# Optimization experiments

Hardware: AMD Instinct MI355X
Metric: run time of the kernel (lower is better)

## Reference

```python
import jax, jax.numpy as jnp
import numpy as np

D_MODEL = 1024
D_FF = 4096
NUM_EXPERTS = 8
TOP_K = 2


def setup_inputs() -> dict:
    key = jax.random.key(0)
    ks = jax.random.split(key, 7)
    s = 1.0 / np.sqrt(D_MODEL)
    sf = 1.0 / np.sqrt(D_FF)
    x = jax.random.normal(ks[0], (4, 2048, D_MODEL), dtype=jnp.float32)
    gate_w = jax.random.uniform(ks[1], (D_MODEL, NUM_EXPERTS), minval=-s, maxval=s, dtype=jnp.float32)
    gate_b = jnp.zeros((NUM_EXPERTS,), dtype=jnp.float32)
    w1 = jax.random.uniform(ks[2], (NUM_EXPERTS, D_MODEL, D_FF), minval=-s, maxval=s, dtype=jnp.float32)
    b1 = jax.random.uniform(ks[3], (NUM_EXPERTS, D_FF), minval=-s, maxval=s, dtype=jnp.float32)
    w2 = jax.random.uniform(ks[4], (NUM_EXPERTS, D_FF, D_MODEL), minval=-sf, maxval=sf, dtype=jnp.float32)
    b2 = jax.random.uniform(ks[5], (NUM_EXPERTS, D_MODEL), minval=-sf, maxval=sf, dtype=jnp.float32)
    return {"x": x, "gate_w": gate_w, "gate_b": gate_b, "w1": w1, "b1": b1, "w2": w2, "b2": b2}


def reference(x, gate_w, gate_b, w1, b1, w2, b2):
    # Router: softmax over experts, then top-k with renormalization.
    router_logits = jnp.einsum('bsd,de->bse', x, gate_w) + gate_b  # [B,S,E]
    router_probs = jax.nn.softmax(router_logits, axis=-1)
    topk_probs, topk_idx = jax.lax.top_k(router_probs, TOP_K)      # [B,S,K]
    topk_probs = topk_probs / jnp.sum(topk_probs, axis=-1, keepdims=True)

    # Dense combine weights: comb[b,s,e] = sum_k topk_probs[b,s,k] * (topk_idx[b,s,k]==e)
    one_hot = jax.nn.one_hot(topk_idx, NUM_EXPERTS, dtype=x.dtype)  # [B,S,K,E]
    comb = jnp.einsum('bsk,bske->bse', topk_probs, one_hot)         # [B,S,E]

    # Loop over the small fixed expert set; weight unselected experts by 0.
    out = jnp.zeros_like(x)
    for e in range(NUM_EXPERTS):
        h = jax.nn.relu(jnp.einsum('bsd,df->bsf', x, w1[e]) + b1[e])
        y = jnp.einsum('bsf,fd->bsd', h, w2[e]) + b2[e]
        out = out + comb[..., e:e + 1] * y

    # Routing statistics (same math as the torch module).
    expert_usage = jnp.mean(one_hot, axis=(0, 1, 2))  # fraction of (token,k) slots per expert
    avg_probs = jnp.mean(router_probs, axis=(0, 1))
    load_balance_loss = jnp.var(avg_probs, ddof=1)    # torch.var is unbiased by default
    return out, expert_usage, load_balance_loss
```

## Files before the change

### kernel.cpp

```cpp
#include <hip/hip_runtime.h>
#include <hip/hip_bf16.h>
#include <stdint.h>

#define D_MODEL 1024
#define D_FF    4096
#define NE      8
#define NTOK    8192
#define OUT_MAIN (NTOK * D_MODEL)

typedef float f32x4 __attribute__((ext_vector_type(4)));
typedef short s16x8 __attribute__((ext_vector_type(8)));

struct __align__(8) bh4 { __hip_bfloat16 x, y, z, w; };

static const size_t OFF_E12  = 4096;
static const size_t OFF_PFR  = 36864;
static const size_t OFF_ATOK = 102400;
static const size_t OFF_AP   = 167936;
static const size_t OFF_XB   = 262144;
static const size_t OFF_W1T  = OFF_XB  + (size_t)NTOK * D_MODEL * 2;
static const size_t OFF_W2T  = OFF_W1T + (size_t)NE * D_MODEL * D_FF * 2;
static const size_t OFF_H    = OFF_W2T + (size_t)NE * D_MODEL * D_FF * 2;

__device__ inline void gll16(const void* g, void* lds) {
  __builtin_amdgcn_global_load_lds((__attribute__((address_space(1))) void*)g,
                                   (__attribute__((address_space(3))) void*)lds,
                                   16, 0, 0);
}

__global__ __launch_bounds__(256) void cvt_transpose_kernel(
    const float* __restrict__ src, __hip_bfloat16* __restrict__ dst, int K, int N)
{
  __shared__ __hip_bfloat16 tile[64][68];
  const int e = blockIdx.z;
  const float* s = src + (size_t)e * K * N;
  __hip_bfloat16* d = dst + (size_t)e * K * N;
  const int n0 = blockIdx.x * 64, k0 = blockIdx.y * 64;
  const int t = threadIdx.x;
#pragma unroll
  for (int i = 0; i < 4; ++i) {
    int q = i * 256 + t;
    int r = q >> 4, c4 = (q & 15) * 4;
    float4 v = *(const float4*)(s + (size_t)(k0 + r) * N + n0 + c4);
    tile[r][c4 + 0] = __float2bfloat16(v.x);
    tile[r][c4 + 1] = __float2bfloat16(v.y);
    tile[r][c4 + 2] = __float2bfloat16(v.z);
    tile[r][c4 + 3] = __float2bfloat16(v.w);
  }
  __syncthreads();
  const int n = t >> 2, c = (t & 3) * 16;
  __align__(16) __hip_bfloat16 tmp[16];
#pragma unroll
  for (int j = 0; j < 16; ++j) tmp[j] = tile[c + j][n];
  uint4* tv = (uint4*)tmp;
  __hip_bfloat16* dp = d + (size_t)(n0 + n) * K + k0 + c;
  ((uint4*)dp)[0] = tv[0];
  ((uint4*)dp)[1] = tv[1];
}

__global__ __launch_bounds__(256) void router_kernel(
    const float* __restrict__ x, const float* __restrict__ gw, const float* __restrict__ gb,
    __hip_bfloat16* __restrict__ xb, int* __restrict__ e12, float2* __restrict__ pfr,
    int* __restrict__ cnt, float* __restrict__ probsum)
{
  const int l = threadIdx.x & 63;
  const int t = blockIdx.x * 4 + (threadIdx.x >> 6);
  const float4* xr = (const float4*)(x + (size_t)t * D_MODEL);
  bh4* xbr = (bh4*)(xb + (size_t)t * D_MODEL);
  float a[8] = {0, 0, 0, 0, 0, 0, 0, 0};
#pragma unroll
  for (int c = 0; c < 4; ++c) {
    int idx = c * 64 + l;
    float4 v = xr[idx];
    bh4 hb;
    hb.x = __float2bfloat16(v.x); hb.y = __float2bfloat16(v.y);
    hb.z = __float2bfloat16(v.z); hb.w = __float2bfloat16(v.w);
    xbr[idx] = hb;
    const float* g = gw + (size_t)idx * 32;
#pragma unroll
    for (int j = 0; j < 4; ++j) {
      float xv = (&v.x)[j];
#pragma unroll
      for (int e = 0; e < 8; ++e) a[e] = fmaf(xv, g[j * 8 + e], a[e]);
    }
  }
#pragma unroll
  for (int e = 0; e < 8; ++e) {
    float s = a[e];
#pragma unroll
    for (int off = 32; off > 0; off >>= 1) s += __shfl_xor(s, off, 64);
    a[e] = s + gb[e];
  }
  float m = a[0];
#pragma unroll
  for (int e = 1; e < 8; ++e) m = fmaxf(m, a[e]);
  float p[8], s = 0.f;
#pragma unroll
  for (int e = 0; e < 8; ++e) { p[e] = expf(a[e] - m); s += p[e]; }
  float inv = 1.0f / s;
#pragma unroll
  for (int e = 0; e < 8; ++e) p[e] *= inv;
  int e1 = 0; float p1 = p[0];
#pragma unroll
  for (int e = 1; e < 8; ++e) if (p[e] > p1) { p1 = p[e]; e1 = e; }
  int e2 = (e1 == 0) ? 1 : 0; float p2 = p[e2];
#pragma unroll
  for (int e = 0; e < 8; ++e) if (e != e1 && p[e] > p2) { p2 = p[e]; e2 = e; }

  if (l < 8) unsafeAtomicAdd(probsum + l, p[l]);
  if (l == 0) {
    float rs = 1.0f / (p1 + p2);
    e12[t] = e1 | (e2 << 8);
    pfr[t] = make_float2(p1 * rs, p2 * rs);
    atomicAdd(cnt + e1, 1);
    atomicAdd(cnt + e2, 1);
  }
}

__global__ void finalize_kernel(int* __restrict__ ctrl, float* __restrict__ probsum,
                                float* __restrict__ out_tail)
{
  if (threadIdx.x != 0) return;
  int off = 0;
  float avg[8]; float mean = 0.f;
#pragma unroll
  for (int e = 0; e < 8; ++e) {
    int c = ctrl[e];
    ctrl[8 + e]  = off;
    ctrl[16 + e] = off;
    off += c;
    out_tail[e] = (float)c * (1.0f / 16384.0f);
    avg[e] = probsum[e] * (1.0f / 8192.0f);
    mean += avg[e];
  }
  mean *= 0.125f;
  float v = 0.f;
#pragma unroll
  for (int e = 0; e < 8; ++e) { float d = avg[e] - mean; v += d * d; }
  out_tail[8] = v * (1.0f / 7.0f);
}

__global__ __launch_bounds__(256) void scatter_kernel(
    const int* __restrict__ e12, const float2* __restrict__ pfr,
    int* __restrict__ cursor, int* __restrict__ atok, float* __restrict__ ap)
{
  int t = blockIdx.x * 256 + threadIdx.x;
  int ee = e12[t];
  float2 p = pfr[t];
  int pos0 = atomicAdd(cursor + (ee & 0xff), 1);
  atok[pos0] = t; ap[pos0] = p.x;
  int pos1 = atomicAdd(cursor + (ee >> 8), 1);
  atok[pos1] = t; ap[pos1] = p.y;
}

template <bool G1>
__global__ __launch_bounds__(256) void moe_gemm_kernel(
    const __hip_bfloat16* __restrict__ A, const __hip_bfloat16* __restrict__ Bw,
    const float* __restrict__ bias, __hip_bfloat16* __restrict__ Hout,
    float* __restrict__ Oout, const int* __restrict__ ctrl,
    const int* __restrict__ atok, const float* __restrict__ ap)
{
  constexpr int KD = G1 ? D_MODEL : D_FF;
  constexpr int ND = G1 ? D_FF : D_MODEL;
  constexpr int KITERS = KD / 64;
  const int e = blockIdx.z;
  const int cte = ctrl[e];
  const int mt = blockIdx.y;
  if (mt * 128 >= cte) return;
  const int n0 = blockIdx.x * 128;
  const int slot0 = ctrl[16 + e] + mt * 128;
  int cntLoc = cte - mt * 128; if (cntLoc > 128) cntLoc = 128;

  __shared__ ushort As[128 * 64];
  __shared__ ushort Bs[128 * 64];

  const int t = threadIdx.x, l = t & 63, w = t >> 6;

  const ushort* ag[4];
  const ushort* bg[4];
#pragma unroll
  for (int i = 0; i < 4; ++i) {
    int q = i * 256 + t;
    int row = q >> 3, cl = q & 7, cg = cl ^ (row & 7);
    int rr = row < cntLoc ? row : 0;
    size_t arow;
    if constexpr (G1) arow = (size_t)atok[slot0 + rr] * D_MODEL;
    else              arow = (size_t)(slot0 + rr) * D_FF;
    ag[i] = (const ushort*)A + arow + cg * 8;
    bg[i] = (const ushort*)Bw + (size_t)e * ND * KD + (size_t)(n0 + row) * KD + cg * 8;
  }

  f32x4 acc[4][4] = {};
  const int wm = w & 1, wn = w >> 1;
  const int ml = l & 15, kg = l >> 4;

  for (int kt = 0; kt < KITERS; ++kt) {
#pragma unroll
    for (int i = 0; i < 4; ++i) {
      gll16(ag[i], &As[(i * 256 + w * 64) * 8]);
      ag[i] += 64;
    }
#pragma unroll
    for (int i = 0; i < 4; ++i) {
      gll16(bg[i], &Bs[(i * 256 + w * 64) * 8]);
      bg[i] += 64;
    }
    __syncthreads();
#pragma unroll
    for (int ks = 0; ks < 2; ++ks) {
      s16x8 af[4], bf[4];
#pragma unroll
      for (int mi = 0; mi < 4; ++mi) {
        int row = wm * 64 + mi * 16 + ml;
        int c = ks * 4 + kg;
        af[mi] = *(const s16x8*)&As[row * 64 + ((c ^ (row & 7)) * 8)];
      }
#pragma unroll
      for (int ni = 0; ni < 4; ++ni) {
        int row = wn * 64 + ni * 16 + ml;
        int c = ks * 4 + kg;
        bf[ni] = *(const s16x8*)&Bs[row * 64 + ((c ^ (row & 7)) * 8)];
      }
#pragma unroll
      for (int mi = 0; mi < 4; ++mi)
#pragma unroll
        for (int ni = 0; ni < 4; ++ni)
          acc[mi][ni] = __builtin_amdgcn_mfma_f32_16x16x32_bf16(af[mi], bf[ni], acc[mi][ni], 0, 0, 0);
    }
    __syncthreads();
  }

  const int lr = kg * 4, lc = ml;
  if constexpr (G1) {
#pragma unroll
    for (int ni = 0; ni < 4; ++ni) {
      int col = n0 + wn * 64 + ni * 16 + lc;
      float bv = bias[(size_t)e * ND + col];
#pragma unroll
      for (int mi = 0; mi < 4; ++mi) {
#pragma unroll
        for (int r = 0; r < 4; ++r) {
          int rl = wm * 64 + mi * 16 + lr + r;
          if (rl < cntLoc) {
            float vv = fmaxf(acc[mi][ni][r] + bv, 0.0f);
            Hout[(size_t)(slot0 + rl) * D_FF + col] = __float2bfloat16(vv);
          }
        }
      }
    }
  } else {
    float bv[4];
#pragma unroll
    for (int ni = 0; ni < 4; ++ni)
      bv[ni] = bias[(size_t)e * ND + n0 + wn * 64 + ni * 16 + lc];
#pragma unroll
    for (int mi = 0; mi < 4; ++mi) {
#pragma unroll
      for (int r = 0; r < 4; ++r) {
        int rl = wm * 64 + mi * 16 + lr + r;
        if (rl < cntLoc) {
          int slot = slot0 + rl;
          float p = ap[slot];
          float* orow = Oout + (size_t)atok[slot] * D_MODEL + n0;
#pragma unroll
          for (int ni = 0; ni < 4; ++ni) {
            int colL = wn * 64 + ni * 16 + lc;
            unsafeAtomicAdd(orow + colL, p * (acc[mi][ni][r] + bv[ni]));
          }
        }
      }
    }
  }
}

extern "C" void kernel_launch(void* const* d_in, const int* in_sizes, int n_in,
                              void* d_out, int out_size, void* d_ws, size_t ws_size,
                              hipStream_t stream)
{
  const float* x  = (const float*)d_in[0];
  const float* gw = (const float*)d_in[1];
  const float* gb = (const float*)d_in[2];
  const float* w1 = (const float*)d_in[3];
  const float* b1 = (const float*)d_in[4];
  const float* w2 = (const float*)d_in[5];
  const float* b2 = (const float*)d_in[6];
  float* out = (float*)d_out;
  char* ws = (char*)d_ws;

  int*    ctrl    = (int*)ws;
  float*  probsum = (float*)ws + 24;
  int*    e12  = (int*)(ws + OFF_E12);
  float2* pfr  = (float2*)(ws + OFF_PFR);
  int*    atok = (int*)(ws + OFF_ATOK);
  float*  ap   = (float*)(ws + OFF_AP);
  __hip_bfloat16* xb   = (__hip_bfloat16*)(ws + OFF_XB);
  __hip_bfloat16* w1t  = (__hip_bfloat16*)(ws + OFF_W1T);
  __hip_bfloat16* w2t  = (__hip_bfloat16*)(ws + OFF_W2T);
  __hip_bfloat16* hbuf = (__hip_bfloat16*)(ws + OFF_H);

  hipMemsetAsync(d_out, 0, (size_t)out_size * sizeof(float), stream);
  hipMemsetAsync(d_ws, 0, 4096, stream);

  cvt_transpose_kernel<<<dim3(D_FF / 64, D_MODEL / 64, NE), 256, 0, stream>>>(w1, w1t, D_MODEL, D_FF);
  cvt_transpose_kernel<<<dim3(D_MODEL / 64, D_FF / 64, NE), 256, 0, stream>>>(w2, w2t, D_FF, D_MODEL);
  router_kernel<<<NTOK / 4, 256, 0, stream>>>(x, gw, gb, xb, e12, pfr, ctrl, probsum);
  finalize_kernel<<<1, 64, 0, stream>>>(ctrl, probsum, out + OUT_MAIN);
  scatter_kernel<<<NTOK / 256, 256, 0, stream>>>(e12, pfr, ctrl + 8, atok, ap);
  moe_gemm_kernel<true ><<<dim3(D_FF / 128, 64, NE), 256, 0, stream>>>(xb, w1t, b1, hbuf, nullptr, ctrl, atok, ap);
  moe_gemm_kernel<false><<<dim3(D_MODEL / 128, 64, NE), 256, 0, stream>>>(hbuf, w2t, b2, nullptr, out, ctrl, atok, ap);
}
```

Before: 1.160 ms.

## Split-K the second expert GEMM and make token scatter deterministic

The down-projection GEMM is split into two K halves, each a separate block that atomically adds into the output, with the bias applied only by the first half. This doubles the block count for the smaller-N GEMM and should improve occupancy. Router statistics now use per-block partial sums, and a ballot-based count/place pass replaces the global atomic scatter, which also removes the workspace memset. The split-K path doubles the atomic traffic to the output in exchange for more parallelism.

```diff
diff --git a/kernel.cpp b/kernel.cpp
--- a/kernel.cpp
+++ b/kernel.cpp
@@ -13,14 +13,14 @@
 
 struct __align__(8) bh4 { __hip_bfloat16 x, y, z, w; };
 
-static const size_t OFF_E12  = 4096;
-static const size_t OFF_PFR  = 36864;
-static const size_t OFF_ATOK = 102400;
-static const size_t OFF_AP   = 167936;
-static const size_t OFF_XB   = 262144;
-static const size_t OFF_W1T  = OFF_XB  + (size_t)NTOK * D_MODEL * 2;
-static const size_t OFF_W2T  = OFF_W1T + (size_t)NE * D_MODEL * D_FF * 2;
-static const size_t OFF_H    = OFF_W2T + (size_t)NE * D_MODEL * D_FF * 2;
+static const size_t OFF_E12   = 4096;
+static const size_t OFF_PFR   = 36864;
+static const size_t OFF_ATOK  = 102400;
+static const size_t OFF_AP    = 167936;
+static const size_t OFF_XB    = 262144;
+static const size_t OFF_W1T   = OFF_XB  + (size_t)NTOK * D_MODEL * 2;
+static const size_t OFF_W2T   = OFF_W1T + (size_t)NE * D_MODEL * D_FF * 2;
+static const size_t OFF_H     = OFF_W2T + (size_t)NE * D_MODEL * D_FF * 2;
 
 __device__ inline void gll16(const void* g, void* lds) {
   __builtin_amdgcn_global_load_lds((__attribute__((address_space(1))) void*)g,
@@ -61,10 +61,12 @@
 __global__ __launch_bounds__(256) void router_kernel(
     const float* __restrict__ x, const float* __restrict__ gw, const float* __restrict__ gb,
     __hip_bfloat16* __restrict__ xb, int* __restrict__ e12, float2* __restrict__ pfr,
-    int* __restrict__ cnt, float* __restrict__ probsum)
-{
+    float* __restrict__ blkps)
+{
+  __shared__ float lps[4][8];
   const int l = threadIdx.x & 63;
-  const int t = blockIdx.x * 4 + (threadIdx.x >> 6);
+  const int w = threadIdx.x >> 6;
+  const int t = blockIdx.x * 4 + w;
   const float4* xr = (const float4*)(x + (size_t)t * D_MODEL);
   bh4* xbr = (bh4*)(xb + (size_t)t * D_MODEL);
   float a[8] = {0, 0, 0, 0, 0, 0, 0, 0};
@@ -107,50 +109,106 @@
 #pragma unroll
   for (int e = 0; e < 8; ++e) if (e != e1 && p[e] > p2) { p2 = p[e]; e2 = e; }
 
-  if (l < 8) unsafeAtomicAdd(probsum + l, p[l]);
+  if (l < 8) lps[w][l] = p[l];
   if (l == 0) {
     float rs = 1.0f / (p1 + p2);
     e12[t] = e1 | (e2 << 8);
     pfr[t] = make_float2(p1 * rs, p2 * rs);
-    atomicAdd(cnt + e1, 1);
-    atomicAdd(cnt + e2, 1);
-  }
-}
-
-__global__ void finalize_kernel(int* __restrict__ ctrl, float* __restrict__ probsum,
-                                float* __restrict__ out_tail)
-{
-  if (threadIdx.x != 0) return;
-  int off = 0;
-  float avg[8]; float mean = 0.f;
-#pragma unroll
-  for (int e = 0; e < 8; ++e) {
-    int c = ctrl[e];
-    ctrl[8 + e]  = off;
-    ctrl[16 + e] = off;
-    off += c;
-    out_tail[e] = (float)c * (1.0f / 16384.0f);
-    avg[e] = probsum[e] * (1.0f / 8192.0f);
-    mean += avg[e];
-  }
-  mean *= 0.125f;
-  float v = 0.f;
-#pragma unroll
-  for (int e = 0; e < 8; ++e) { float d = avg[e] - mean; v += d * d; }
-  out_tail[8] = v * (1.0f / 7.0f);
-}
-
-__global__ __launch_bounds__(256) void scatter_kernel(
-    const int* __restrict__ e12, const float2* __restrict__ pfr,
-    int* __restrict__ cursor, int* __restrict__ atok, float* __restrict__ ap)
-{
-  int t = blockIdx.x * 256 + threadIdx.x;
-  int ee = e12[t];
-  float2 p = pfr[t];
-  int pos0 = atomicAdd(cursor + (ee & 0xff), 1);
-  atok[pos0] = t; ap[pos0] = p.x;
-  int pos1 = atomicAdd(cursor + (ee >> 8), 1);
-  atok[pos1] = t; ap[pos1] = p.y;
+  }
+  __syncthreads();
+  if (threadIdx.x < 8)
+    blkps[(size_t)blockIdx.x * 8 + threadIdx.x] =
+        lps[0][threadIdx.x] + lps[1][threadIdx.x] + lps[2][threadIdx.x] + lps[3][threadIdx.x];
+}
+
+__global__ __launch_bounds__(256) void count_kernel(
+    const int* __restrict__ e12, int* __restrict__ sblkcnt)
+{
+  __shared__ int wcnt[4][8];
+  const int t = threadIdx.x, b = blockIdx.x, w = t >> 6, l = t & 63;
+  int ee = e12[b * 256 + t];
+  int e1 = ee & 0xff, e2 = ee >> 8;
+#pragma unroll
+  for (int k = 0; k < 8; ++k) {
+    unsigned long long c1 = __ballot(e1 == k);
+    unsigned long long c2 = __ballot(e2 == k);
+    if (l == 0) wcnt[w][k] = __popcll(c1) + __popcll(c2);
+  }
+  __syncthreads();
+  if (t < 8) sblkcnt[b * 8 + t] = wcnt[0][t] + wcnt[1][t] + wcnt[2][t] + wcnt[3][t];
+}
+
+__global__ __launch_bounds__(256) void finalize_kernel(
+    int* __restrict__ ctrl, const float* __restrict__ blkps, const int* __restrict__ sblkcnt,
+    int* __restrict__ bases, float* __restrict__ out_tail)
+{
+  __shared__ float part[256];
+  __shared__ float ps[8];
+  __shared__ int scnt[8];
+  const int t = threadIdx.x;
+  const int e = t & 7, ch = t >> 3;
+  float s = 0.f;
+  for (int i = 0; i < 64; ++i) s += blkps[(size_t)(ch * 64 + i) * 8 + e];
+  part[t] = s;
+  __syncthreads();
+  if (t < 8) {
+    float a = 0.f;
+    for (int c = 0; c < 32; ++c) a += part[c * 8 + t];
+    ps[t] = a;
+    int cn = 0;
+    for (int b = 0; b < 32; ++b) cn += sblkcnt[b * 8 + t];
+    scnt[t] = cn;
+    ctrl[t] = cn;
+    out_tail[t] = (float)cn * (1.0f / 16384.0f);
+  }
+  __syncthreads();
+  if (t < 8) {
+    int eo = 0;
+    for (int i = 0; i < t; ++i) eo += scnt[i];
+    ctrl[16 + t] = eo;
+    int run = eo;
+    for (int b = 0; b < 32; ++b) { bases[b * 8 + t] = run; run += sblkcnt[b * 8 + t]; }
+    if (t == 0) {
+      float mean = 0.f;
+      for (int i = 0; i < 8; ++i) mean += ps[i];
+      mean *= (1.0f / 8192.0f) * 0.125f;
+      float v = 0.f;
+      for (int i = 0; i < 8; ++i) { float d = ps[i] * (1.0f / 8192.0f) - mean; v += d * d; }
+      out_tail[8] = v * (1.0f / 7.0f);
+    }
+  }
+}
+
+__global__ __launch_bounds__(256) void place_kernel(
+    const int* __restrict__ e12, const float2* __restrict__ pfr, const int* __restrict__ bases,
+    int* __restrict__ atok, float* __restrict__ ap)
+{
+  __shared__ int wcnt[4][8];
+  const int t = threadIdx.x, b = blockIdx.x, w = t >> 6, l = t & 63;
+  int tok = b * 256 + t;
+  int ee = e12[tok];
+  int e1 = ee & 0xff, e2 = ee >> 8;
+  float2 p = pfr[tok];
+  unsigned long long myA = 0, myA2 = 0, myB = 0;
+#pragma unroll
+  for (int k = 0; k < 8; ++k) {
+    unsigned long long c1 = __ballot(e1 == k);
+    unsigned long long c2 = __ballot(e2 == k);
+    if (k == e1) myA = c1;
+    if (k == e2) { myA2 = c1; myB = c2; }
+    if (l == 0) wcnt[w][k] = __popcll(c1) + __popcll(c2);
+  }
+  __syncthreads();
+  int base1 = bases[b * 8 + e1];
+  int base2 = bases[b * 8 + e2];
+  for (int w2 = 0; w2 < 4; ++w2) {
+    if (w2 < w) { base1 += wcnt[w2][e1]; base2 += wcnt[w2][e2]; }
+  }
+  unsigned long long below = ((unsigned long long)1 << l) - 1;
+  int pos1 = base1 + __popcll(myA & below);
+  int pos2 = base2 + __popcll(myA2) + __popcll(myB & below);
+  atok[pos1] = tok; ap[pos1] = p.x;
+  atok[pos2] = tok; ap[pos2] = p.y;
 }
 
 template <bool G1>
@@ -162,10 +220,12 @@
 {
   constexpr int KD = G1 ? D_MODEL : D_FF;
   constexpr int ND = G1 ? D_FF : D_MODEL;
-  constexpr int KITERS = KD / 64;
+  constexpr int KRUN = G1 ? (KD / 64) : (KD / 128);
   const int e = blockIdx.z;
   const int cte = ctrl[e];
-  const int mt = blockIdx.y;
+  int mt, ks;
+  if constexpr (G1) { mt = blockIdx.y; ks = 0; }
+  else              { mt = blockIdx.y >> 1; ks = blockIdx.y & 1; }
   if (mt * 128 >= cte) return;
   const int n0 = blockIdx.x * 128;
   const int slot0 = ctrl[16 + e] + mt * 128;
@@ -175,6 +235,7 @@
   __shared__ ushort Bs[128 * 64];
 
   const int t = threadIdx.x, l = t & 63, w = t >> 6;
+  const int kbase = ks * (KD / 2);
 
   const ushort* ag[4];
   const ushort* bg[4];
@@ -186,15 +247,15 @@
     size_t arow;
     if constexpr (G1) arow = (size_t)atok[slot0 + rr] * D_MODEL;
     else              arow = (size_t)(slot0 + rr) * D_FF;
-    ag[i] = (const ushort*)A + arow + cg * 8;
-    bg[i] = (const ushort*)Bw + (size_t)e * ND * KD + (size_t)(n0 + row) * KD + cg * 8;
+    ag[i] = (const ushort*)A + arow + kbase + cg * 8;
+    bg[i] = (const ushort*)Bw + (size_t)e * ND * KD + (size_t)(n0 + row) * KD + kbase + cg * 8;
   }
 
   f32x4 acc[4][4] = {};
   const int wm = w & 1, wn = w >> 1;
   const int ml = l & 15, kg = l >> 4;
 
-  for (int kt = 0; kt < KITERS; ++kt) {
+  for (int kt = 0; kt < KRUN; ++kt) {
 #pragma unroll
     for (int i = 0; i < 4; ++i) {
       gll16(ag[i], &As[(i * 256 + w * 64) * 8]);
@@ -207,18 +268,18 @@
     }
     __syncthreads();
 #pragma unroll
-    for (int ks = 0; ks < 2; ++ks) {
+    for (int kss = 0; kss < 2; ++kss) {
       s16x8 af[4], bf[4];
 #pragma unroll
       for (int mi = 0; mi < 4; ++mi) {
         int row = wm * 64 + mi * 16 + ml;
-        int c = ks * 4 + kg;
+        int c = kss * 4 + kg;
         af[mi] = *(const s16x8*)&As[row * 64 + ((c ^ (row & 7)) * 8)];
       }
 #pragma unroll
       for (int ni = 0; ni < 4; ++ni) {
         int row = wn * 64 + ni * 16 + ml;
-        int c = ks * 4 + kg;
+        int c = kss * 4 + kg;
         bf[ni] = *(const s16x8*)&Bs[row * 64 + ((c ^ (row & 7)) * 8)];
       }
 #pragma unroll
@@ -252,7 +313,7 @@
     float bv[4];
 #pragma unroll
     for (int ni = 0; ni < 4; ++ni)
-      bv[ni] = bias[(size_t)e * ND + n0 + wn * 64 + ni * 16 + lc];
+      bv[ni] = (ks == 0) ? bias[(size_t)e * ND + n0 + wn * 64 + ni * 16 + lc] : 0.0f;
 #pragma unroll
     for (int mi = 0; mi < 4; ++mi) {
 #pragma unroll
@@ -288,7 +349,8 @@
   char* ws = (char*)d_ws;
 
   int*    ctrl    = (int*)ws;
-  float*  probsum = (float*)ws + 24;
+  int*    bases   = (int*)(ws + 1024);
+  int*    sblkcnt = (int*)(ws + 3072);
   int*    e12  = (int*)(ws + OFF_E12);
   float2* pfr  = (float2*)(ws + OFF_PFR);
   int*    atok = (int*)(ws + OFF_ATOK);
@@ -297,15 +359,16 @@
   __hip_bfloat16* w1t  = (__hip_bfloat16*)(ws + OFF_W1T);
   __hip_bfloat16* w2t  = (__hip_bfloat16*)(ws + OFF_W2T);
   __hip_bfloat16* hbuf = (__hip_bfloat16*)(ws + OFF_H);
+  float*  blkps = (float*)(ws + OFF_H);
 
   hipMemsetAsync(d_out, 0, (size_t)out_size * sizeof(float), stream);
-  hipMemsetAsync(d_ws, 0, 4096, stream);
 
   cvt_transpose_kernel<<<dim3(D_FF / 64, D_MODEL / 64, NE), 256, 0, stream>>>(w1, w1t, D_MODEL, D_FF);
   cvt_transpose_kernel<<<dim3(D_MODEL / 64, D_FF / 64, NE), 256, 0, stream>>>(w2, w2t, D_FF, D_MODEL);
-  router_kernel<<<NTOK / 4, 256, 0, stream>>>(x, gw, gb, xb, e12, pfr, ctrl, probsum);
-  finalize_kernel<<<1, 64, 0, stream>>>(ctrl, probsum, out + OUT_MAIN);
-  scatter_kernel<<<NTOK / 256, 256, 0, stream>>>(e12, pfr, ctrl + 8, atok, ap);
+  router_kernel<<<NTOK / 4, 256, 0, stream>>>(x, gw, gb, xb, e12, pfr, blkps);
+  count_kernel<<<NTOK / 256, 256, 0, stream>>>(e12, sblkcnt);
+  finalize_kernel<<<1, 256, 0, stream>>>(ctrl, blkps, sblkcnt, bases, out + OUT_MAIN);
+  place_kernel<<<NTOK / 256, 256, 0, stream>>>(e12, pfr, bases, atok, ap);
   moe_gemm_kernel<true ><<<dim3(D_FF / 128, 64, NE), 256, 0, stream>>>(xb, w1t, b1, hbuf, nullptr, ctrl, atok, ap);
-  moe_gemm_kernel<false><<<dim3(D_MODEL / 128, 64, NE), 256, 0, stream>>>(hbuf, w2t, b2, nullptr, out, ctrl, atok, ap);
-}
+  moe_gemm_kernel<false><<<dim3(D_MODEL / 128, 128, NE), 256, 0, stream>>>(hbuf, w2t, b2, nullptr, out, ctrl, atok, ap);
+}
```

Measured after the change: 932.1 us. 19.6% less time.
